# Kernel optimization log

Hardware: AMD Instinct MI355X
Metric: run time of the kernel (lower is better)

Reference implementation:

```python
import jax, jax.numpy as jnp
import numpy as np

B, L, D, A = 64, 196, 2048, 1024  # batch, locations, hidden_size, att_hid_size


def setup_inputs() -> dict:
    key = jax.random.key(0)
    ks = jax.random.split(key, 8)
    scale = 0.02
    return {
        "att_features": jax.random.normal(ks[0], (B, L, D), dtype=jnp.float32),
        "h": jax.random.normal(ks[1], (B, D), dtype=jnp.float32),
        "W_att": jax.random.normal(ks[2], (D, A), dtype=jnp.float32) * scale,
        "b_att": jnp.zeros((A,), dtype=jnp.float32),
        "W_h": jax.random.normal(ks[3], (D, A), dtype=jnp.float32) * scale,
        "b_h": jnp.zeros((A,), dtype=jnp.float32),
        "w_alpha": jax.random.normal(ks[4], (A, 1), dtype=jnp.float32) * scale,
        "b_alpha": jnp.zeros((1,), dtype=jnp.float32),
    }


def reference(att_features, h, W_att, b_att, W_h, b_h, w_alpha, b_alpha):
    b = att_features.shape[0]
    d = att_features.shape[-1]
    locations = att_features.size // b // d
    af = att_features.reshape(b, locations, d)            # [B, L, D]
    p_att = af @ W_att + b_att                            # [B, L, A]
    p_h = (h @ W_h + b_h)[:, None, :]                     # [B, 1, A]
    scores = (jnp.tanh(p_att + p_h) @ w_alpha + b_alpha)[..., 0]  # [B, L]
    weights = jax.nn.softmax(scores, axis=1)              # [B, L]
    weighted = jnp.einsum('bl,bld->bd', weights, af)      # [B, D]
    return weighted, weights
```

## Files before the change

kernel.cpp:

```cpp
#include <hip/hip_runtime.h>


typedef unsigned short u16;
typedef u16 u16x8 __attribute__((ext_vector_type(8)));
typedef __bf16 bf16x8 __attribute__((ext_vector_type(8)));
typedef float f32x4 __attribute__((ext_vector_type(4)));

#define B_ 64
#define L_ 196
#define D_ 2048
#define A_ 1024
#define M_ (B_ * L_)

__device__ __forceinline__ u16 f2bf(float x) {
  unsigned u = __float_as_uint(x);
  unsigned r = (u + 0x7fffu + ((u >> 16) & 1u)) >> 16;
  return (u16)r;
}

__device__ __forceinline__ float tanh_fast(float x) {
  float e = __expf(2.0f * x);
  return 1.0f - 2.0f / (e + 1.0f);
}

__device__ __forceinline__ void gload_lds16(const void* g, void* l) {
  __builtin_amdgcn_global_load_lds(
      (const __attribute__((address_space(1))) void*)g,
      (__attribute__((address_space(3))) void*)l, 16, 0, 0);
}

__global__ __launch_bounds__(256) void prep_k(
    const float* __restrict__ af, u16* __restrict__ afb,
    const float* __restrict__ W, u16* __restrict__ WT,
    const float* __restrict__ h, const float* __restrict__ Wh,
    float* __restrict__ ph) {
  __shared__ float smem[2112];
  const int bid = blockIdx.x;
  const int t = threadIdx.x;
  if (bid < 256) {
    const int ag = bid & 3, bg = (bid >> 2) & 7, dc = bid >> 5;
    const int d0 = dc * 256;
    for (int i = t; i < 2048; i += 256)
      smem[i] = h[(size_t)(bg * 8 + (i >> 8)) * D_ + d0 + (i & 255)];
    __syncthreads();
    const int a = ag * 256 + t;
    float acc[8] = {};
#pragma unroll 8
    for (int d = 0; d < 256; ++d) {
      float wv = Wh[(size_t)(d0 + d) * A_ + a];
#pragma unroll
      for (int bb = 0; bb < 8; ++bb) acc[bb] += smem[bb * 256 + d] * wv;
    }
#pragma unroll
    for (int bb = 0; bb < 8; ++bb)
      atomicAdd(&ph[(size_t)(bg * 8 + bb) * A_ + a], acc[bb]);
  } else if (bid < 2304) {
    const int tb = bid - 256;
    const int n0 = (tb & 31) * 32, k0 = (tb >> 5) * 32;
    const int tx = t & 31, ty = t >> 5;
    float (*tt)[33] = (float (*)[33])smem;
#pragma unroll
    for (int i = 0; i < 4; ++i)
      tt[ty + i * 8][tx] = W[(size_t)(k0 + ty + i * 8) * A_ + n0 + tx];
    __syncthreads();
#pragma unroll
    for (int i = 0; i < 4; ++i)
      WT[(size_t)(n0 + ty + i * 8) * D_ + k0 + tx] = f2bf(tt[tx][ty + i * 8]);
  } else {
    const int cb = bid - 2304;
    const size_t n = (size_t)M_ * D_;
    for (size_t e = ((size_t)cb * 256 + t) * 8; e < n;
         e += (size_t)2048 * 256 * 8) {
      float4 v0 = *(const float4*)(af + e);
      float4 v1 = *(const float4*)(af + e + 4);
      u16x8 p;
      p[0] = f2bf(v0.x); p[1] = f2bf(v0.y); p[2] = f2bf(v0.z); p[3] = f2bf(v0.w);
      p[4] = f2bf(v1.x); p[5] = f2bf(v1.y); p[6] = f2bf(v1.z); p[7] = f2bf(v1.w);
      *(u16x8*)(afb + e) = p;
    }
  }
}

__global__ __launch_bounds__(512, 2) void gemm8_k(
    const u16* __restrict__ afb, const u16* __restrict__ WT,
    const float* __restrict__ ph, const float* __restrict__ batt,
    const float* __restrict__ bh, const float* __restrict__ walpha,
    float* __restrict__ scores4) {
  __shared__ __align__(16) u16 As[2][2][8192];
  __shared__ __align__(16) u16 Bs[2][2][8192];
  const int tid = threadIdx.x;
  const int lane = tid & 63;
  const int wid = tid >> 6;
  const int wr = wid >> 2;
  const int wc = wid & 3;
  const int wchalf = wc >> 1, wcl = wc & 1;
  const int fr = lane & 15, fq = lane >> 4;

  const int xcd = blockIdx.x & 7, idx = blockIdx.x >> 3;
  const int wg = (xcd < 4 ? xcd * 25 : 100 + (xcd - 4) * 24) + idx;
  const int m0 = (wg >> 2) * 256;
  const int n0 = (wg & 3) * 256;

  int rowc[2], colc[2];
#pragma unroll
  for (int r = 0; r < 2; ++r) {
    int c = r * 512 + tid;
    int s = c >> 6, cw = c & 63;
    rowc[r] = (s >> 1) * 16 + (cw >> 2);
    colc[r] = (s & 1) * 32 + ((((cw & 3) * 16) ^ (((cw >> 5) & 1) * 32)) >> 1);
  }
  const u16* srcA[2][2];
  const u16* srcB[2][2];
#pragma unroll
  for (int hh = 0; hh < 2; ++hh)
#pragma unroll
    for (int r = 0; r < 2; ++r) {
      srcA[hh][r] = afb + (size_t)(m0 + hh * 128 + rowc[r]) * D_ + colc[r];
      srcB[hh][r] = WT + (size_t)(n0 + hh * 128 + rowc[r]) * D_ + colc[r];
    }

  const int laneA = (lane & 15) * 64 + (((lane >> 4) * 16) ^ ((lane & 8) << 2));

  f32x4 acc[8][4] = {};
  u16x8 areg[4][2], breg[4][2];

#define STG_A(BUF, H, KT)                                                    \
  do {                                                                       \
    gload_lds16(srcA[H][0] + (size_t)(KT) * 64, &As[BUF][H][wid * 512]);     \
    gload_lds16(srcA[H][1] + (size_t)(KT) * 64, &As[BUF][H][4096 + wid * 512]); \
  } while (0)
#define STG_B(BUF, H, KT)                                                    \
  do {                                                                       \
    gload_lds16(srcB[H][0] + (size_t)(KT) * 64, &Bs[BUF][H][wid * 512]);     \
    gload_lds16(srcB[H][1] + (size_t)(KT) * 64, &Bs[BUF][H][4096 + wid * 512]); \
  } while (0)
#define LDA_HALF(BF, MH)                                                     \
  do {                                                                       \
    _Pragma("unroll") for (int q = 0; q < 4; ++q) {                          \
      areg[q][0] = *(const u16x8*)&As[BF][wr][((((MH)*4 + q) * 2 + 0) * 1024 + laneA) >> 1]; \
      areg[q][1] = *(const u16x8*)&As[BF][wr][((((MH)*4 + q) * 2 + 1) * 1024 + laneA) >> 1]; \
    }                                                                        \
  } while (0)
#define LDB_PAIR(BF, NQ)                                                     \
  do {                                                                       \
    _Pragma("unroll") for (int nn = 0; nn < 2; ++nn) {                       \
      breg[(NQ)*2 + nn][0] = *(const u16x8*)&Bs[BF][wchalf][(((wcl * 4 + (NQ)*2 + nn) * 2 + 0) * 1024 + laneA) >> 1]; \
      breg[(NQ)*2 + nn][1] = *(const u16x8*)&Bs[BF][wchalf][(((wcl * 4 + (NQ)*2 + nn) * 2 + 1) * 1024 + laneA) >> 1]; \
    }                                                                        \
  } while (0)
#define MM_QUAD(MH, NQ)                                                      \
  do {                                                                       \
    _Pragma("unroll") for (int q = 0; q < 4; ++q)                            \
    _Pragma("unroll") for (int nn = 0; nn < 2; ++nn)                         \
    _Pragma("unroll") for (int kh = 0; kh < 2; ++kh)                         \
      acc[(MH)*4 + q][(NQ)*2 + nn] = __builtin_amdgcn_mfma_f32_16x16x32_bf16( \
          __builtin_bit_cast(bf16x8, areg[q][kh]),                           \
          __builtin_bit_cast(bf16x8, breg[(NQ)*2 + nn][kh]),                 \
          acc[(MH)*4 + q][(NQ)*2 + nn], 0, 0, 0);                            \
  } while (0)
#define PH_PRE()                                                             \
  do {                                                                       \
    __builtin_amdgcn_s_barrier();                                            \
    asm volatile("s_waitcnt lgkmcnt(0)" ::: "memory");                       \
    __builtin_amdgcn_s_setprio(1);                                           \
  } while (0)
#define PH_POST()                                                            \
  do {                                                                       \
    __builtin_amdgcn_s_setprio(0);                                           \
    __builtin_amdgcn_s_barrier();                                            \
  } while (0)
#define KTILE(BF, T, MODE)                                                   \
  do {                                                                       \
    LDA_HALF(BF, 0); LDB_PAIR(BF, 0);                                        \
    if ((MODE) <= 1) STG_A((BF) ^ 1, 1, (T) + 1);                            \
    PH_PRE(); MM_QUAD(0, 0); PH_POST();                                      \
    LDB_PAIR(BF, 1);                                                         \
    PH_PRE(); MM_QUAD(0, 1); PH_POST();                                      \
    LDA_HALF(BF, 1);                                                         \
    if ((MODE) == 0) { STG_B(BF, 0, (T) + 2); STG_B(BF, 1, (T) + 2); }       \
    PH_PRE(); MM_QUAD(1, 0); PH_POST();                                      \
    if ((MODE) == 0) STG_A(BF, 0, (T) + 2);                                  \
    PH_PRE(); MM_QUAD(1, 1);                                                 \
    __builtin_amdgcn_s_setprio(0);                                           \
    if ((MODE) == 0) asm volatile("s_waitcnt vmcnt(6)" ::: "memory");        \
    if ((MODE) == 1) asm volatile("s_waitcnt vmcnt(0)" ::: "memory");        \
    __builtin_amdgcn_s_barrier();                                            \
  } while (0)

  STG_B(0, 0, 0); STG_B(0, 1, 0); STG_A(0, 0, 0); STG_A(0, 1, 0);
  STG_B(1, 0, 1); STG_B(1, 1, 1); STG_A(1, 0, 1);
  asm volatile("s_waitcnt vmcnt(6)" ::: "memory");
  __builtin_amdgcn_s_barrier();

#pragma unroll 1
  for (int it = 0; it < 15; ++it) {
    const int t = it * 2;
    KTILE(0, t, 0);
    KTILE(1, t + 1, 0);
  }
  KTILE(0, 30, 1);
  KTILE(1, 31, 2);

  const int gnb = n0 + wc * 64 + fr;
  float wa[4], bsv[4], p0[4], p1[4], p2[4];
  const int b0 = m0 / L_;
  const int s1 = (b0 + 1) * L_, s2 = (b0 + 2) * L_;
  const int b1 = (b0 + 1 > 63) ? 63 : b0 + 1;
  const int b2 = (b0 + 2 > 63) ? 63 : b0 + 2;
#pragma unroll
  for (int ni = 0; ni < 4; ++ni) {
    const int gn = gnb + ni * 16;
    wa[ni] = walpha[gn];
    bsv[ni] = batt[gn] + bh[gn];
    p0[ni] = ph[(size_t)b0 * A_ + gn];
    p1[ni] = ph[(size_t)b1 * A_ + gn];
    p2[ni] = ph[(size_t)b2 * A_ + gn];
  }
  float (*redp)[128][4] = (float (*)[128][4])As;
#pragma unroll
  for (int mi = 0; mi < 8; ++mi) {
#pragma unroll
    for (int rr = 0; rr < 4; ++rr) {
      const int lr = mi * 16 + fq * 4 + rr;
      const int gm = m0 + wr * 128 + lr;
      float sp = 0.f;
#pragma unroll
      for (int ni = 0; ni < 4; ++ni) {
        const float pv = (gm >= s2) ? p2[ni] : ((gm >= s1) ? p1[ni] : p0[ni]);
        const float p = acc[mi][ni][rr] + pv + bsv[ni];
        sp += tanh_fast(p) * wa[ni];
      }
      sp += __shfl_xor(sp, 1);
      sp += __shfl_xor(sp, 2);
      sp += __shfl_xor(sp, 4);
      sp += __shfl_xor(sp, 8);
      if (fr == 0) redp[wr][lr][wc] = sp;
    }
  }
  __syncthreads();
  if (tid < 256) {
    f32x4 v = ((const f32x4*)redp)[tid];
    scores4[(size_t)(n0 >> 8) * M_ + m0 + tid] = v[0] + v[1] + v[2] + v[3];
  }
}

__global__ __launch_bounds__(256) void softmax_k(const float* __restrict__ s4,
                                                 float* __restrict__ wout) {
  __shared__ float red[4];
  int b = blockIdx.x, t = threadIdx.x;
  float s = -1e30f;
  if (t < L_) {
    const int i = b * L_ + t;
    s = s4[i] + s4[M_ + i] + s4[2 * M_ + i] + s4[3 * M_ + i];
  }
  float m = s;
#pragma unroll
  for (int o = 32; o; o >>= 1) m = fmaxf(m, __shfl_xor(m, o));
  if ((t & 63) == 0) red[t >> 6] = m;
  __syncthreads();
  m = fmaxf(fmaxf(red[0], red[1]), fmaxf(red[2], red[3]));
  float e = (t < L_) ? __expf(s - m) : 0.f;
  float sum = e;
#pragma unroll
  for (int o = 32; o; o >>= 1) sum += __shfl_xor(sum, o);
  __syncthreads();
  if ((t & 63) == 0) red[t >> 6] = sum;
  __syncthreads();
  sum = red[0] + red[1] + red[2] + red[3];
  if (t < L_) wout[b * L_ + t] = e / sum;
}

__global__ __launch_bounds__(256) void wsum_k(const u16* __restrict__ afb,
                                              const float* __restrict__ w,
                                              float* __restrict__ out) {
  __shared__ float wl[256];
  __shared__ float part[256][8];
  int b = blockIdx.y;
  int lq = threadIdx.x >> 6;
  int dl = threadIdx.x & 63;
  int d8 = blockIdx.x * 64 + dl;
  wl[threadIdx.x] = (threadIdx.x < L_) ? w[b * L_ + threadIdx.x] : 0.f;
  __syncthreads();
  float acc[8] = {};
  for (int l = lq * 49; l < lq * 49 + 49; ++l) {
    u16x8 v = *(const u16x8*)(afb + (size_t)(b * L_ + l) * D_ + d8 * 8);
    float ww = wl[l];
#pragma unroll
    for (int j = 0; j < 8; ++j)
      acc[j] += ww * __uint_as_float((unsigned)v[j] << 16);
  }
#pragma unroll
  for (int j = 0; j < 8; ++j) part[threadIdx.x][j] = acc[j];
  __syncthreads();
  if (threadIdx.x < 64) {
    float4 o0, o1;
    o0.x = part[dl][0] + part[64 + dl][0] + part[128 + dl][0] + part[192 + dl][0];
    o0.y = part[dl][1] + part[64 + dl][1] + part[128 + dl][1] + part[192 + dl][1];
    o0.z = part[dl][2] + part[64 + dl][2] + part[128 + dl][2] + part[192 + dl][2];
    o0.w = part[dl][3] + part[64 + dl][3] + part[128 + dl][3] + part[192 + dl][3];
    o1.x = part[dl][4] + part[64 + dl][4] + part[128 + dl][4] + part[192 + dl][4];
    o1.y = part[dl][5] + part[64 + dl][5] + part[128 + dl][5] + part[192 + dl][5];
    o1.z = part[dl][6] + part[64 + dl][6] + part[128 + dl][6] + part[192 + dl][6];
    o1.w = part[dl][7] + part[64 + dl][7] + part[128 + dl][7] + part[192 + dl][7];
    *(float4*)(out + (size_t)b * D_ + d8 * 8) = o0;
    *(float4*)(out + (size_t)b * D_ + d8 * 8 + 4) = o1;
  }
}

extern "C" void kernel_launch(void* const* d_in, const int* in_sizes, int n_in,
                              void* d_out, int out_size, void* d_ws, size_t ws_size,
                              hipStream_t stream) {
  const float* af    = (const float*)d_in[0];
  const float* h     = (const float*)d_in[1];
  const float* W_att = (const float*)d_in[2];
  const float* b_att = (const float*)d_in[3];
  const float* W_h   = (const float*)d_in[4];
  const float* b_h   = (const float*)d_in[5];
  const float* w_al  = (const float*)d_in[6];
  float* out = (float*)d_out;
  char* ws = (char*)d_ws;

  u16* afb       = (u16*)ws;
  u16* WT        = (u16*)(ws + 0x3200000);
  float* ph      = (float*)(ws + 0x3600000);
  float* scores4 = (float*)(ws + 0x3640000);

  hipMemsetAsync(ph, 0, 256u << 10, stream);
  prep_k<<<4352, 256, 0, stream>>>(af, afb, W_att, WT, h, W_h, ph);
  gemm8_k<<<196, 512, 0, stream>>>(afb, WT, ph, b_att, b_h, w_al, scores4);
  softmax_k<<<64, 256, 0, stream>>>(scores4, out + (size_t)B_ * D_);
  wsum_k<<<dim3(4, 64), 256, 0, stream>>>(afb, out + (size_t)B_ * D_, out);
}
```

Measured before the change: 123.8 us.

## Merge GEMM K-tile phases and fuse softmax into weighted-sum kernel

The GEMM K-tile loop now issues both B-pair LDS loads up front and runs two MFMA quads per barrier-delimited phase, halving the number of barrier/priority phases per tile. The final barrier is also skipped on the last tile. Softmax is folded into the weighted-sum kernel, where each of the 4 D-blocks recomputes the per-batch softmax and only block 0 writes the weights, removing one launch. This trades redundant softmax work and higher register pressure from holding more B fragments for fewer syncs and launches.

```diff
diff --git a/kernel.cpp b/kernel.cpp
--- a/kernel.cpp
+++ b/kernel.cpp
@@ -171,20 +171,17 @@
   } while (0)
 #define KTILE(BF, T, MODE)                                                   \
   do {                                                                       \
-    LDA_HALF(BF, 0); LDB_PAIR(BF, 0);                                        \
+    LDA_HALF(BF, 0); LDB_PAIR(BF, 0); LDB_PAIR(BF, 1);                       \
     if ((MODE) <= 1) STG_A((BF) ^ 1, 1, (T) + 1);                            \
-    PH_PRE(); MM_QUAD(0, 0); PH_POST();                                      \
-    LDB_PAIR(BF, 1);                                                         \
-    PH_PRE(); MM_QUAD(0, 1); PH_POST();                                      \
+    PH_PRE(); MM_QUAD(0, 0); MM_QUAD(0, 1); PH_POST();                       \
     LDA_HALF(BF, 1);                                                         \
-    if ((MODE) == 0) { STG_B(BF, 0, (T) + 2); STG_B(BF, 1, (T) + 2); }       \
-    PH_PRE(); MM_QUAD(1, 0); PH_POST();                                      \
-    if ((MODE) == 0) STG_A(BF, 0, (T) + 2);                                  \
-    PH_PRE(); MM_QUAD(1, 1);                                                 \
+    if ((MODE) == 0) { STG_B(BF, 0, (T) + 2); STG_B(BF, 1, (T) + 2);         \
+                       STG_A(BF, 0, (T) + 2); }                              \
+    PH_PRE(); MM_QUAD(1, 0); MM_QUAD(1, 1);                                  \
     __builtin_amdgcn_s_setprio(0);                                           \
     if ((MODE) == 0) asm volatile("s_waitcnt vmcnt(6)" ::: "memory");        \
     if ((MODE) == 1) asm volatile("s_waitcnt vmcnt(0)" ::: "memory");        \
-    __builtin_amdgcn_s_barrier();                                            \
+    if ((MODE) <= 1) __builtin_amdgcn_s_barrier();                           \
   } while (0)
 
   STG_B(0, 0, 0); STG_B(0, 1, 0); STG_A(0, 0, 0); STG_A(0, 1, 0);
@@ -244,10 +241,15 @@
   }
 }
 
-__global__ __launch_bounds__(256) void softmax_k(const float* __restrict__ s4,
-                                                 float* __restrict__ wout) {
+__global__ __launch_bounds__(256) void wsum_sm_k(const u16* __restrict__ afb,
+                                                 const float* __restrict__ s4,
+                                                 float* __restrict__ out) {
+  __shared__ float wl[256];
+  __shared__ float part[256][8];
   __shared__ float red[4];
-  int b = blockIdx.x, t = threadIdx.x;
+  const int b = blockIdx.y;
+  const int t = threadIdx.x;
+
   float s = -1e30f;
   if (t < L_) {
     const int i = b * L_ + t;
@@ -267,20 +269,14 @@
   if ((t & 63) == 0) red[t >> 6] = sum;
   __syncthreads();
   sum = red[0] + red[1] + red[2] + red[3];
-  if (t < L_) wout[b * L_ + t] = e / sum;
-}
-
-__global__ __launch_bounds__(256) void wsum_k(const u16* __restrict__ afb,
-                                              const float* __restrict__ w,
-                                              float* __restrict__ out) {
-  __shared__ float wl[256];
-  __shared__ float part[256][8];
-  int b = blockIdx.y;
-  int lq = threadIdx.x >> 6;
-  int dl = threadIdx.x & 63;
-  int d8 = blockIdx.x * 64 + dl;
-  wl[threadIdx.x] = (threadIdx.x < L_) ? w[b * L_ + threadIdx.x] : 0.f;
-  __syncthreads();
+  const float w = e / sum;
+  wl[t] = w;
+  if (t < L_ && blockIdx.x == 0) out[(size_t)B_ * D_ + b * L_ + t] = w;
+  __syncthreads();
+
+  const int lq = t >> 6;
+  const int dl = t & 63;
+  const int d8 = blockIdx.x * 64 + dl;
   float acc[8] = {};
   for (int l = lq * 49; l < lq * 49 + 49; ++l) {
     u16x8 v = *(const u16x8*)(afb + (size_t)(b * L_ + l) * D_ + d8 * 8);
@@ -290,9 +286,9 @@
       acc[j] += ww * __uint_as_float((unsigned)v[j] << 16);
   }
 #pragma unroll
-  for (int j = 0; j < 8; ++j) part[threadIdx.x][j] = acc[j];
-  __syncthreads();
-  if (threadIdx.x < 64) {
+  for (int j = 0; j < 8; ++j) part[t][j] = acc[j];
+  __syncthreads();
+  if (t < 64) {
     float4 o0, o1;
     o0.x = part[dl][0] + part[64 + dl][0] + part[128 + dl][0] + part[192 + dl][0];
     o0.y = part[dl][1] + part[64 + dl][1] + part[128 + dl][1] + part[192 + dl][1];
@@ -328,6 +324,5 @@
   hipMemsetAsync(ph, 0, 256u << 10, stream);
   prep_k<<<4352, 256, 0, stream>>>(af, afb, W_att, WT, h, W_h, ph);
   gemm8_k<<<196, 512, 0, stream>>>(afb, WT, ph, b_att, b_h, w_al, scores4);
-  softmax_k<<<64, 256, 0, stream>>>(scores4, out + (size_t)B_ * D_);
-  wsum_k<<<dim3(4, 64), 256, 0, stream>>>(afb, out + (size_t)B_ * D_, out);
-}
+  wsum_sm_k<<<dim3(4, 64), 256, 0, stream>>>(afb, scores4, out);
+}
```

Measured after the change: 119.2 us. 3.7% less time.
